# Performance work log

Measured on AMD Instinct MI355X. Metric: run time of the kernel, lower is better.

## Reference

```python
import jax, jax.numpy as jnp
import numpy as np

Q_MAX = 127.0  # 8-bit, narrow range [-127, 127] (pytorch-quantization default)


def fake_quant(x, amax):
    """Fake quantization with clipped-STE semantics (matches pytorch-quantization).

    amax may be a scalar (per-tensor) or broadcastable (per-channel). Treated as
    a constant (stop_gradient'd by caller where appropriate).
    """
    amax = jnp.maximum(amax, 1e-12)
    scale = amax / Q_MAX
    xq = jnp.round(jnp.clip(x / scale, -Q_MAX, Q_MAX)) * scale
    xc = jnp.clip(x, -amax, amax)  # identity grad inside range, zero outside
    return xc + jax.lax.stop_gradient(xq - xc)


def quant_conv1x1(x, w, b):
    """QuantConv2d with 1x1 kernel: fake-quant input (per-tensor dynamic max amax)
    and weight (per-output-channel max amax), then conv + bias.
    x: [B,C,H,W], w: [O,C], b: [O]
    """
    a_amax = jax.lax.stop_gradient(jnp.max(jnp.abs(x)))
    xq = fake_quant(x, a_amax)
    w_amax = jax.lax.stop_gradient(jnp.max(jnp.abs(w), axis=1, keepdims=True))
    wq = fake_quant(w, w_amax)
    y = jnp.einsum('bchw,oc->bohw', xq, wq)
    return y + b[None, :, None, None]


def setup_inputs() -> dict:
    key = jax.random.key(0)
    k1, k2, k3, k4 = jax.random.split(key, 4)
    B, C, Cr, H, W = 64, 32, 8, 128, 128
    x = jax.random.normal(k1, (B, C, H, W), dtype=jnp.float32)
    identity = jax.random.normal(k2, (B, C, H, W), dtype=jnp.float32)
    w_reduce = jax.random.normal(k3, (Cr, C), dtype=jnp.float32) * 0.1
    b_reduce = jnp.zeros((Cr,), dtype=jnp.float32)
    w_expand = jax.random.normal(k4, (C, Cr), dtype=jnp.float32) * 0.1
    b_expand = jnp.zeros((C,), dtype=jnp.float32)
    return {"x": x, "identity": identity,
            "w_reduce": w_reduce, "b_reduce": b_reduce,
            "w_expand": w_expand, "b_expand": b_expand}


def reference(x, identity, w_reduce, b_reduce, w_expand, b_expand):
    h = quant_conv1x1(x, w_reduce, b_reduce)      # [B,8,H,W]
    h = h * jax.nn.sigmoid(h)                     # SiLU
    g = quant_conv1x1(h, w_expand, b_expand)      # [B,32,H,W]
    return identity * jax.nn.sigmoid(g)
```

## Files before the change

### kernel.cpp

```cpp
#include <hip/hip_runtime.h>
#include <hip/hip_cooperative_groups.h>
#include <math.h>

namespace cg = cooperative_groups;

#define QMAX 127.0f
#define CIN 32
#define CR 8
#define HW 16384
#define BATCH 64
#define NPIX (BATCH*HW)
#define NQUAD (NPIX/4)
#define NX (BATCH*CIN*HW)
#define COOP_BLOCKS (NQUAD/256)

#define H_OFF 64
#define WS_NEEDED ((size_t)(H_OFF + (size_t)NPIX * CR) * 4)

__device__ __forceinline__ float fq(float v, float inv_scale, float scale) {
    return rintf(fminf(fmaxf(v * inv_scale, -QMAX), QMAX)) * scale;
}
__device__ __forceinline__ float sigmoidf_(float v) {
    return __builtin_amdgcn_rcpf(1.0f + __expf(-v));
}

__global__ __launch_bounds__(256, 4) void se_fused(const float* __restrict__ x,
                                                   const float* __restrict__ identity,
                                                   const float* __restrict__ wr,
                                                   const float* __restrict__ br,
                                                   const float* __restrict__ we,
                                                   const float* __restrict__ be,
                                                   unsigned int* __restrict__ wsu,
                                                   float* __restrict__ out) {
    cg::grid_group grid = cg::this_grid();
    int t = threadIdx.x;
    __shared__ float wqr[CR * CIN], wqe[CIN * CR], bsh[CR], besh[CIN], amr[CR], ame[CIN];
    __shared__ float red[4];

    if (t < CR) {
        float mm = 0.f;
        for (int c = 0; c < CIN; c++) mm = fmaxf(mm, fabsf(wr[t * CIN + c]));
        amr[t] = fmaxf(mm, 1e-12f);
        bsh[t] = br[t];
    }
    if (t >= 64 && t < 64 + CIN) {
        int r = t - 64;
        float mm = 0.f;
        for (int c = 0; c < CR; c++) mm = fmaxf(mm, fabsf(we[r * CR + c]));
        ame[r] = fmaxf(mm, 1e-12f);
        besh[r] = be[r];
    }
    __syncthreads();
    {
        float a1 = amr[t >> 5];
        wqr[t] = fq(wr[t], QMAX / a1, a1 * (1.f / QMAX));
        float a2 = ame[t >> 3];
        wqe[t] = fq(we[t], QMAX / a2, a2 * (1.f / QMAX));
    }
    __syncthreads();

    const int tid = blockIdx.x * 256 + t;

    {
        const float4* x4 = (const float4*)x;
        float m = 0.f;
#pragma unroll 8
        for (int i = 0; i < 32; i++) {
            float4 v = x4[tid + i * NQUAD];
            m = fmaxf(m, fmaxf(fmaxf(fabsf(v.x), fabsf(v.y)), fmaxf(fabsf(v.z), fabsf(v.w))));
        }
#pragma unroll
        for (int off = 32; off > 0; off >>= 1) m = fmaxf(m, __shfl_xor(m, off, 64));
        if ((t & 63) == 0) red[t >> 6] = m;
        __syncthreads();
        if (t == 0) {
            m = fmaxf(fmaxf(red[0], red[1]), fmaxf(red[2], red[3]));
            atomicMax(&wsu[0], __float_as_uint(m));
        }
    }
    grid.sync();

    float a_amax = fmaxf(__uint_as_float(
        __hip_atomic_load(&wsu[0], __ATOMIC_ACQUIRE, __HIP_MEMORY_SCOPE_AGENT)), 1e-12f);
    float ascale = a_amax * (1.f / QMAX), ainv = QMAX / a_amax;
    const int b = tid >> 12;
    const int hw = (tid & 4095) << 2;
    const size_t base = (size_t)b * CIN * HW + hw;
    float h[CR][4];
    {
        float hacc[CR][4];
#pragma unroll
        for (int o = 0; o < CR; o++)
#pragma unroll
            for (int v = 0; v < 4; v++) hacc[o][v] = 0.f;
        const float* xb = x + base;
#pragma unroll
        for (int c = 0; c < CIN; c++) {
            float4 xv = *(const float4*)(xb + (size_t)c * HW);
            float q0 = fq(xv.x, ainv, ascale), q1 = fq(xv.y, ainv, ascale);
            float q2 = fq(xv.z, ainv, ascale), q3 = fq(xv.w, ainv, ascale);
#pragma unroll
            for (int o = 0; o < CR; o++) {
                float w = wqr[o * CIN + c];
                hacc[o][0] += q0 * w; hacc[o][1] += q1 * w;
                hacc[o][2] += q2 * w; hacc[o][3] += q3 * w;
            }
        }
        float m = 0.f;
#pragma unroll
        for (int o = 0; o < CR; o++) {
            float bb = bsh[o];
#pragma unroll
            for (int v = 0; v < 4; v++) {
                float hv = hacc[o][v] + bb;
                hv = hv * sigmoidf_(hv);
                h[o][v] = hv;
                m = fmaxf(m, fabsf(hv));
            }
        }
#pragma unroll
        for (int off = 32; off > 0; off >>= 1) m = fmaxf(m, __shfl_xor(m, off, 64));
        __syncthreads();
        if ((t & 63) == 0) red[t >> 6] = m;
        __syncthreads();
        if (t == 0) {
            m = fmaxf(fmaxf(red[0], red[1]), fmaxf(red[2], red[3]));
            atomicMax(&wsu[1], __float_as_uint(m));
        }
    }
    grid.sync();

    float h_amax = fmaxf(__uint_as_float(
        __hip_atomic_load(&wsu[1], __ATOMIC_ACQUIRE, __HIP_MEMORY_SCOPE_AGENT)), 1e-12f);
    float hscale = h_amax * (1.f / QMAX), hinv = QMAX / h_amax;
#pragma unroll
    for (int o = 0; o < CR; o++)
#pragma unroll
        for (int v = 0; v < 4; v++) h[o][v] = fq(h[o][v], hinv, hscale);

#pragma unroll 4
    for (int o2 = 0; o2 < CIN; o2++) {
        float g0 = besh[o2], g1 = g0, g2 = g0, g3 = g0;
#pragma unroll
        for (int cr = 0; cr < CR; cr++) {
            float w = wqe[o2 * CR + cr];
            g0 += h[cr][0] * w; g1 += h[cr][1] * w;
            g2 += h[cr][2] * w; g3 += h[cr][3] * w;
        }
        size_t off = base + (size_t)o2 * HW;
        float4 idv = *(const float4*)(identity + off);
        float4 ov;
        ov.x = idv.x * sigmoidf_(g0);
        ov.y = idv.y * sigmoidf_(g1);
        ov.z = idv.z * sigmoidf_(g2);
        ov.w = idv.w * sigmoidf_(g3);
        *(float4*)(out + off) = ov;
    }
}

__global__ __launch_bounds__(256) void k1_xmax(const float4* __restrict__ x4,
                                               unsigned int* __restrict__ wsu) {
    int idx = blockIdx.x * 256 + threadIdx.x;
    float m = 0.f;
#pragma unroll
    for (int i = 0; i < 16; i++) {
        float4 v = x4[idx + i * 524288];
        m = fmaxf(m, fmaxf(fmaxf(fabsf(v.x), fabsf(v.y)), fmaxf(fabsf(v.z), fabsf(v.w))));
    }
#pragma unroll
    for (int off = 32; off > 0; off >>= 1) m = fmaxf(m, __shfl_xor(m, off, 64));
    __shared__ float red[4];
    int t = threadIdx.x;
    if ((t & 63) == 0) red[t >> 6] = m;
    __syncthreads();
    if (t == 0) {
        m = fmaxf(fmaxf(red[0], red[1]), fmaxf(red[2], red[3]));
        atomicMax(&wsu[0], __float_as_uint(m));
    }
}

__global__ __launch_bounds__(256) void k2_hmax(const float* __restrict__ x,
                                               const float* __restrict__ wr,
                                               const float* __restrict__ br,
                                               const unsigned int* __restrict__ wsu,
                                               unsigned int* __restrict__ hmax,
                                               float* __restrict__ hbuf) {
    __shared__ float wq[CR * CIN], bsh[CR], amr[CR];
    int t = threadIdx.x;
    if (t < CR) {
        float mm = 0.f;
        for (int c = 0; c < CIN; c++) mm = fmaxf(mm, fabsf(wr[t * CIN + c]));
        amr[t] = fmaxf(mm, 1e-12f);
        bsh[t] = br[t];
    }
    __syncthreads();
    {
        float amax = amr[t >> 5];
        wq[t] = fq(wr[t], QMAX / amax, amax * (1.f / QMAX));
    }
    __syncthreads();
    float a_amax = fmaxf(__uint_as_float(wsu[0]), 1e-12f);
    float scale = a_amax * (1.f / QMAX), inv_scale = QMAX / a_amax;
    int tid = blockIdx.x * 256 + t;
    int b = tid >> 12;
    int hw = (tid & 4095) << 2;
    const float* xb = x + (size_t)b * CIN * HW + hw;
    float hacc[CR][4];
#pragma unroll
    for (int o = 0; o < CR; o++)
#pragma unroll
        for (int v = 0; v < 4; v++) hacc[o][v] = 0.f;
#pragma unroll
    for (int c = 0; c < CIN; c++) {
        float4 xv = *(const float4*)(xb + (size_t)c * HW);
        float q0 = fq(xv.x, inv_scale, scale), q1 = fq(xv.y, inv_scale, scale);
        float q2 = fq(xv.z, inv_scale, scale), q3 = fq(xv.w, inv_scale, scale);
#pragma unroll
        for (int o = 0; o < CR; o++) {
            float w = wq[o * CIN + c];
            hacc[o][0] += q0 * w; hacc[o][1] += q1 * w;
            hacc[o][2] += q2 * w; hacc[o][3] += q3 * w;
        }
    }
    float m = 0.f;
#pragma unroll
    for (int o = 0; o < CR; o++) {
        float bb = bsh[o];
        float4 hv;
        float* hp = (float*)&hv;
#pragma unroll
        for (int v = 0; v < 4; v++) {
            float h = hacc[o][v] + bb;
            h = h * sigmoidf_(h);
            hp[v] = h;
            m = fmaxf(m, fabsf(h));
        }
        if (hbuf) *(float4*)(hbuf + ((size_t)(b * CR + o)) * HW + hw) = hv;
    }
#pragma unroll
    for (int off = 32; off > 0; off >>= 1) m = fmaxf(m, __shfl_xor(m, off, 64));
    __shared__ float red[4];
    if ((t & 63) == 0) red[t >> 6] = m;
    __syncthreads();
    if (t == 0) {
        m = fmaxf(fmaxf(red[0], red[1]), fmaxf(red[2], red[3]));
        atomicMax(hmax, __float_as_uint(m));
    }
}

__global__ __launch_bounds__(256) void k3_out(const float* __restrict__ hbuf,
                                              const float* __restrict__ identity,
                                              const float* __restrict__ we,
                                              const float* __restrict__ be,
                                              const unsigned int* __restrict__ wsu,
                                              float* __restrict__ out) {
    const int y = blockIdx.y;
    __shared__ float wqe[16 * CR], besh[16], ame[16];
    int t = threadIdx.x;
    if (t < 16) {
        int r = 16 * y + t;
        float mm = 0.f;
        for (int c = 0; c < CR; c++) mm = fmaxf(mm, fabsf(we[r * CR + c]));
        ame[t] = fmaxf(mm, 1e-12f);
        besh[t] = be[r];
    }
    __syncthreads();
    if (t < 128) {
        int r16 = t >> 3;
        float amax = ame[r16];
        wqe[t] = fq(we[(16 * y + r16) * CR + (t & 7)], QMAX / amax, amax * (1.f / QMAX));
    }
    __syncthreads();
    float h_amax = fmaxf(__uint_as_float(wsu[1]), 1e-12f);
    float hscale = h_amax * (1.f / QMAX), hinv = QMAX / h_amax;
    int tid = blockIdx.x * 256 + t;
    int b = tid >> 12;
    int hw = (tid & 4095) << 2;
    size_t base = (size_t)b * CIN * HW + hw;
    float hq[CR][4];
#pragma unroll
    for (int cr = 0; cr < CR; cr++) {
        float4 hv = *(const float4*)(hbuf + ((size_t)(b * CR + cr)) * HW + hw);
        hq[cr][0] = fq(hv.x, hinv, hscale);
        hq[cr][1] = fq(hv.y, hinv, hscale);
        hq[cr][2] = fq(hv.z, hinv, hscale);
        hq[cr][3] = fq(hv.w, hinv, hscale);
    }
#pragma unroll 4
    for (int o = 0; o < 16; o++) {
        float g0 = besh[o], g1 = g0, g2 = g0, g3 = g0;
#pragma unroll
        for (int cr = 0; cr < CR; cr++) {
            float w = wqe[o * CR + cr];
            g0 += hq[cr][0] * w; g1 += hq[cr][1] * w;
            g2 += hq[cr][2] * w; g3 += hq[cr][3] * w;
        }
        size_t off = base + (size_t)(16 * y + o) * HW;
        float4 idv = *(const float4*)(identity + off);
        float4 ov;
        ov.x = idv.x * sigmoidf_(g0);
        ov.y = idv.y * sigmoidf_(g1);
        ov.z = idv.z * sigmoidf_(g2);
        ov.w = idv.w * sigmoidf_(g3);
        *(float4*)(out + off) = ov;
    }
}

__global__ __launch_bounds__(256) void k3_out_rc(const float* __restrict__ x,
                                                 const float* __restrict__ identity,
                                                 const float* __restrict__ wr,
                                                 const float* __restrict__ br,
                                                 const float* __restrict__ we,
                                                 const float* __restrict__ be,
                                                 const unsigned int* __restrict__ wsu,
                                                 float* __restrict__ out) {
    __shared__ float wqr[CR * CIN], wqe[CIN * CR], bsh[CR], besh[CIN], amr[CR], ame[CIN];
    int t = threadIdx.x;
    if (t < CR) {
        float mm = 0.f;
        for (int c = 0; c < CIN; c++) mm = fmaxf(mm, fabsf(wr[t * CIN + c]));
        amr[t] = fmaxf(mm, 1e-12f);
        bsh[t] = br[t];
    }
    if (t >= 64 && t < 64 + CIN) {
        int r = t - 64;
        float mm = 0.f;
        for (int c = 0; c < CR; c++) mm = fmaxf(mm, fabsf(we[r * CR + c]));
        ame[r] = fmaxf(mm, 1e-12f);
        besh[r] = be[r];
    }
    __syncthreads();
    {
        float amax = amr[t >> 5];
        wqr[t] = fq(wr[t], QMAX / amax, amax * (1.f / QMAX));
        float amax2 = ame[t >> 3];
        wqe[t] = fq(we[t], QMAX / amax2, amax2 * (1.f / QMAX));
    }
    __syncthreads();
    float a_amax = fmaxf(__uint_as_float(wsu[0]), 1e-12f);
    float ascale = a_amax * (1.f / QMAX), ainv = QMAX / a_amax;
    float h_amax = fmaxf(__uint_as_float(wsu[1]), 1e-12f);
    float hscale = h_amax * (1.f / QMAX), hinv = QMAX / h_amax;
    int tid = blockIdx.x * 256 + t;
    int b = tid >> 12;
    int hw = (tid & 4095) << 2;
    size_t base = (size_t)b * CIN * HW + hw;
    const float* xb = x + base;
    float hq[CR][4];
    {
        float hacc[CR][4];
#pragma unroll
        for (int o = 0; o < CR; o++)
#pragma unroll
            for (int v = 0; v < 4; v++) hacc[o][v] = 0.f;
#pragma unroll
        for (int c = 0; c < CIN; c++) {
            float4 xv = *(const float4*)(xb + (size_t)c * HW);
            float q0 = fq(xv.x, ainv, ascale), q1 = fq(xv.y, ainv, ascale);
            float q2 = fq(xv.z, ainv, ascale), q3 = fq(xv.w, ainv, ascale);
#pragma unroll
            for (int o = 0; o < CR; o++) {
                float w = wqr[o * CIN + c];
                hacc[o][0] += q0 * w; hacc[o][1] += q1 * w;
                hacc[o][2] += q2 * w; hacc[o][3] += q3 * w;
            }
        }
#pragma unroll
        for (int o = 0; o < CR; o++) {
            float bb = bsh[o];
#pragma unroll
            for (int v = 0; v < 4; v++) {
                float h = hacc[o][v] + bb;
                h = h * sigmoidf_(h);
                hq[o][v] = fq(h, hinv, hscale);
            }
        }
    }
#pragma unroll 4
    for (int o2 = 0; o2 < CIN; o2++) {
        float g0 = besh[o2], g1 = g0, g2 = g0, g3 = g0;
#pragma unroll
        for (int cr = 0; cr < CR; cr++) {
            float w = wqe[o2 * CR + cr];
            g0 += hq[cr][0] * w; g1 += hq[cr][1] * w;
            g2 += hq[cr][2] * w; g3 += hq[cr][3] * w;
        }
        size_t off = base + (size_t)o2 * HW;
        float4 idv = *(const float4*)(identity + off);
        float4 ov;
        ov.x = idv.x * sigmoidf_(g0);
        ov.y = idv.y * sigmoidf_(g1);
        ov.z = idv.z * sigmoidf_(g2);
        ov.w = idv.w * sigmoidf_(g3);
        *(float4*)(out + off) = ov;
    }
}

extern "C" void kernel_launch(void* const* d_in, const int* in_sizes, int n_in,
                              void* d_out, int out_size, void* d_ws, size_t ws_size,
                              hipStream_t stream) {
    const float* x        = (const float*)d_in[0];
    const float* identity = (const float*)d_in[1];
    const float* wr       = (const float*)d_in[2];
    const float* br       = (const float*)d_in[3];
    const float* we       = (const float*)d_in[4];
    const float* be       = (const float*)d_in[5];
    float* out            = (float*)d_out;
    float* wsf            = (float*)d_ws;
    unsigned int* wsu     = (unsigned int*)d_ws;

    hipMemsetAsync(d_ws, 0, 16, stream);

    int maxb = 0;
    hipError_t qerr = hipOccupancyMaxActiveBlocksPerMultiprocessor(&maxb, se_fused, 256, 0);
    bool coop_ok = false;
    if (qerr == hipSuccess && maxb >= 4) {
        void* args[] = {(void*)&x, (void*)&identity, (void*)&wr, (void*)&br,
                        (void*)&we, (void*)&be, (void*)&wsu, (void*)&out};
        hipError_t lerr = hipLaunchCooperativeKernel((void*)se_fused, dim3(COOP_BLOCKS),
                                                     dim3(256), args, 0, stream);
        coop_ok = (lerr == hipSuccess);
    }
    if (coop_ok) return;

    const bool big_ws = (ws_size >= WS_NEEDED);
    float* hbuf = big_ws ? (wsf + H_OFF) : nullptr;
    hipLaunchKernelGGL(k1_xmax, dim3(2048), dim3(256), 0, stream, (const float4*)x, wsu);
    hipLaunchKernelGGL(k2_hmax, dim3(NQUAD / 256), dim3(256), 0, stream,
                       x, wr, br, wsu, &wsu[1], hbuf);
    if (big_ws) {
        hipLaunchKernelGGL(k3_out, dim3(NQUAD / 256, 2), dim3(256), 0, stream,
                           hbuf, identity, we, be, wsu, out);
    } else {
        hipLaunchKernelGGL(k3_out_rc, dim3(NQUAD / 256), dim3(256), 0, stream,
                           x, identity, wr, br, we, be, wsu, out);
    }
}
```

Measured before the change: 374.6 us.

## Replace cooperative fused kernel with three-kernel pipeline using batched loads and nontemporal IO

Removes the cooperative single-kernel path with two grid syncs and always runs the three-kernel path (x max, h compute/max, output). Each kernel now issues its global loads in a batch behind a scheduling barrier to raise memory-level parallelism. Threads cover two pixels instead of four, which doubles the grid. The output kernel handles all 32 channels in one block and uses nontemporal loads for identity and nontemporal stores for out. In exchange it pays for extra launches and an h round trip through the workspace.

```diff
diff --git a/kernel.cpp b/kernel.cpp
--- a/kernel.cpp
+++ b/kernel.cpp
@@ -1,8 +1,5 @@
 #include <hip/hip_runtime.h>
-#include <hip/hip_cooperative_groups.h>
 #include <math.h>
-
-namespace cg = cooperative_groups;
 
 #define QMAX 127.0f
 #define CIN 32
@@ -10,163 +7,41 @@
 #define HW 16384
 #define BATCH 64
 #define NPIX (BATCH*HW)
+#define NPAIR (NPIX/2)
 #define NQUAD (NPIX/4)
 #define NX (BATCH*CIN*HW)
-#define COOP_BLOCKS (NQUAD/256)
 
 #define H_OFF 64
 #define WS_NEEDED ((size_t)(H_OFF + (size_t)NPIX * CR) * 4)
 
+typedef float v2f __attribute__((ext_vector_type(2)));
+
 __device__ __forceinline__ float fq(float v, float inv_scale, float scale) {
     return rintf(fminf(fmaxf(v * inv_scale, -QMAX), QMAX)) * scale;
 }
 __device__ __forceinline__ float sigmoidf_(float v) {
     return __builtin_amdgcn_rcpf(1.0f + __expf(-v));
 }
-
-__global__ __launch_bounds__(256, 4) void se_fused(const float* __restrict__ x,
-                                                   const float* __restrict__ identity,
-                                                   const float* __restrict__ wr,
-                                                   const float* __restrict__ br,
-                                                   const float* __restrict__ we,
-                                                   const float* __restrict__ be,
-                                                   unsigned int* __restrict__ wsu,
-                                                   float* __restrict__ out) {
-    cg::grid_group grid = cg::this_grid();
-    int t = threadIdx.x;
-    __shared__ float wqr[CR * CIN], wqe[CIN * CR], bsh[CR], besh[CIN], amr[CR], ame[CIN];
-    __shared__ float red[4];
-
-    if (t < CR) {
-        float mm = 0.f;
-        for (int c = 0; c < CIN; c++) mm = fmaxf(mm, fabsf(wr[t * CIN + c]));
-        amr[t] = fmaxf(mm, 1e-12f);
-        bsh[t] = br[t];
-    }
-    if (t >= 64 && t < 64 + CIN) {
-        int r = t - 64;
-        float mm = 0.f;
-        for (int c = 0; c < CR; c++) mm = fmaxf(mm, fabsf(we[r * CR + c]));
-        ame[r] = fmaxf(mm, 1e-12f);
-        besh[r] = be[r];
-    }
-    __syncthreads();
-    {
-        float a1 = amr[t >> 5];
-        wqr[t] = fq(wr[t], QMAX / a1, a1 * (1.f / QMAX));
-        float a2 = ame[t >> 3];
-        wqe[t] = fq(we[t], QMAX / a2, a2 * (1.f / QMAX));
-    }
-    __syncthreads();
-
-    const int tid = blockIdx.x * 256 + t;
-
-    {
-        const float4* x4 = (const float4*)x;
-        float m = 0.f;
-#pragma unroll 8
-        for (int i = 0; i < 32; i++) {
-            float4 v = x4[tid + i * NQUAD];
-            m = fmaxf(m, fmaxf(fmaxf(fabsf(v.x), fabsf(v.y)), fmaxf(fabsf(v.z), fabsf(v.w))));
-        }
-#pragma unroll
-        for (int off = 32; off > 0; off >>= 1) m = fmaxf(m, __shfl_xor(m, off, 64));
-        if ((t & 63) == 0) red[t >> 6] = m;
-        __syncthreads();
-        if (t == 0) {
-            m = fmaxf(fmaxf(red[0], red[1]), fmaxf(red[2], red[3]));
-            atomicMax(&wsu[0], __float_as_uint(m));
-        }
-    }
-    grid.sync();
-
-    float a_amax = fmaxf(__uint_as_float(
-        __hip_atomic_load(&wsu[0], __ATOMIC_ACQUIRE, __HIP_MEMORY_SCOPE_AGENT)), 1e-12f);
-    float ascale = a_amax * (1.f / QMAX), ainv = QMAX / a_amax;
-    const int b = tid >> 12;
-    const int hw = (tid & 4095) << 2;
-    const size_t base = (size_t)b * CIN * HW + hw;
-    float h[CR][4];
-    {
-        float hacc[CR][4];
-#pragma unroll
-        for (int o = 0; o < CR; o++)
-#pragma unroll
-            for (int v = 0; v < 4; v++) hacc[o][v] = 0.f;
-        const float* xb = x + base;
-#pragma unroll
-        for (int c = 0; c < CIN; c++) {
-            float4 xv = *(const float4*)(xb + (size_t)c * HW);
-            float q0 = fq(xv.x, ainv, ascale), q1 = fq(xv.y, ainv, ascale);
-            float q2 = fq(xv.z, ainv, ascale), q3 = fq(xv.w, ainv, ascale);
-#pragma unroll
-            for (int o = 0; o < CR; o++) {
-                float w = wqr[o * CIN + c];
-                hacc[o][0] += q0 * w; hacc[o][1] += q1 * w;
-                hacc[o][2] += q2 * w; hacc[o][3] += q3 * w;
-            }
-        }
-        float m = 0.f;
-#pragma unroll
-        for (int o = 0; o < CR; o++) {
-            float bb = bsh[o];
-#pragma unroll
-            for (int v = 0; v < 4; v++) {
-                float hv = hacc[o][v] + bb;
-                hv = hv * sigmoidf_(hv);
-                h[o][v] = hv;
-                m = fmaxf(m, fabsf(hv));
-            }
-        }
-#pragma unroll
-        for (int off = 32; off > 0; off >>= 1) m = fmaxf(m, __shfl_xor(m, off, 64));
-        __syncthreads();
-        if ((t & 63) == 0) red[t >> 6] = m;
-        __syncthreads();
-        if (t == 0) {
-            m = fmaxf(fmaxf(red[0], red[1]), fmaxf(red[2], red[3]));
-            atomicMax(&wsu[1], __float_as_uint(m));
-        }
-    }
-    grid.sync();
-
-    float h_amax = fmaxf(__uint_as_float(
-        __hip_atomic_load(&wsu[1], __ATOMIC_ACQUIRE, __HIP_MEMORY_SCOPE_AGENT)), 1e-12f);
-    float hscale = h_amax * (1.f / QMAX), hinv = QMAX / h_amax;
-#pragma unroll
-    for (int o = 0; o < CR; o++)
-#pragma unroll
-        for (int v = 0; v < 4; v++) h[o][v] = fq(h[o][v], hinv, hscale);
-
-#pragma unroll 4
-    for (int o2 = 0; o2 < CIN; o2++) {
-        float g0 = besh[o2], g1 = g0, g2 = g0, g3 = g0;
-#pragma unroll
-        for (int cr = 0; cr < CR; cr++) {
-            float w = wqe[o2 * CR + cr];
-            g0 += h[cr][0] * w; g1 += h[cr][1] * w;
-            g2 += h[cr][2] * w; g3 += h[cr][3] * w;
-        }
-        size_t off = base + (size_t)o2 * HW;
-        float4 idv = *(const float4*)(identity + off);
-        float4 ov;
-        ov.x = idv.x * sigmoidf_(g0);
-        ov.y = idv.y * sigmoidf_(g1);
-        ov.z = idv.z * sigmoidf_(g2);
-        ov.w = idv.w * sigmoidf_(g3);
-        *(float4*)(out + off) = ov;
-    }
+__device__ __forceinline__ v2f nt_load2(const float* p) {
+    return __builtin_nontemporal_load((const v2f*)p);
+}
+__device__ __forceinline__ void nt_store2(float* p, float a, float b) {
+    v2f v; v.x = a; v.y = b;
+    __builtin_nontemporal_store(v, (v2f*)p);
 }
 
 __global__ __launch_bounds__(256) void k1_xmax(const float4* __restrict__ x4,
                                                unsigned int* __restrict__ wsu) {
     int idx = blockIdx.x * 256 + threadIdx.x;
+    float4 v[8];
+#pragma unroll
+    for (int i = 0; i < 8; i++) v[i] = x4[idx + i * 1048576];
+    __builtin_amdgcn_sched_barrier(0);
     float m = 0.f;
 #pragma unroll
-    for (int i = 0; i < 16; i++) {
-        float4 v = x4[idx + i * 524288];
-        m = fmaxf(m, fmaxf(fmaxf(fabsf(v.x), fabsf(v.y)), fmaxf(fabsf(v.z), fabsf(v.w))));
-    }
+    for (int i = 0; i < 8; i++)
+        m = fmaxf(m, fmaxf(fmaxf(fabsf(v[i].x), fabsf(v[i].y)),
+                           fmaxf(fabsf(v[i].z), fabsf(v[i].w))));
 #pragma unroll
     for (int off = 32; off > 0; off >>= 1) m = fmaxf(m, __shfl_xor(m, off, 64));
     __shared__ float red[4];
@@ -200,42 +75,53 @@
     }
     __syncthreads();
     float a_amax = fmaxf(__uint_as_float(wsu[0]), 1e-12f);
-    float scale = a_amax * (1.f / QMAX), inv_scale = QMAX / a_amax;
+    float ascale = a_amax * (1.f / QMAX), ainv = QMAX / a_amax;
+
     int tid = blockIdx.x * 256 + t;
-    int b = tid >> 12;
-    int hw = (tid & 4095) << 2;
+    int b = tid >> 13;
+    int hw = (tid & 8191) << 1;
     const float* xb = x + (size_t)b * CIN * HW + hw;
-    float hacc[CR][4];
-#pragma unroll
-    for (int o = 0; o < CR; o++)
-#pragma unroll
-        for (int v = 0; v < 4; v++) hacc[o][v] = 0.f;
-#pragma unroll
-    for (int c = 0; c < CIN; c++) {
-        float4 xv = *(const float4*)(xb + (size_t)c * HW);
-        float q0 = fq(xv.x, inv_scale, scale), q1 = fq(xv.y, inv_scale, scale);
-        float q2 = fq(xv.z, inv_scale, scale), q3 = fq(xv.w, inv_scale, scale);
-#pragma unroll
-        for (int o = 0; o < CR; o++) {
-            float w = wq[o * CIN + c];
-            hacc[o][0] += q0 * w; hacc[o][1] += q1 * w;
-            hacc[o][2] += q2 * w; hacc[o][3] += q3 * w;
-        }
-    }
+
+    float hacc[CR][2];
+#pragma unroll
+    for (int o = 0; o < CR; o++) { hacc[o][0] = 0.f; hacc[o][1] = 0.f; }
+
+#pragma unroll
+    for (int s = 0; s < 2; s++) {
+        float2 xv[16];
+#pragma unroll
+        for (int j = 0; j < 16; j++)
+            xv[j] = *(const float2*)(xb + (size_t)(s * 16 + j) * HW);
+        __builtin_amdgcn_sched_barrier(0);
+#pragma unroll
+        for (int j4 = 0; j4 < 4; j4++) {
+            float q0[4], q1[4];
+#pragma unroll
+            for (int k = 0; k < 4; k++) {
+                q0[k] = fq(xv[j4 * 4 + k].x, ainv, ascale);
+                q1[k] = fq(xv[j4 * 4 + k].y, ainv, ascale);
+            }
+            int c0 = s * 16 + j4 * 4;
+#pragma unroll
+            for (int o = 0; o < CR; o++) {
+                float4 wv = *(const float4*)&wq[o * CIN + c0];
+                hacc[o][0] += q0[0]*wv.x + q0[1]*wv.y + q0[2]*wv.z + q0[3]*wv.w;
+                hacc[o][1] += q1[0]*wv.x + q1[1]*wv.y + q1[2]*wv.z + q1[3]*wv.w;
+            }
+        }
+    }
+
     float m = 0.f;
 #pragma unroll
     for (int o = 0; o < CR; o++) {
         float bb = bsh[o];
-        float4 hv;
-        float* hp = (float*)&hv;
-#pragma unroll
-        for (int v = 0; v < 4; v++) {
-            float h = hacc[o][v] + bb;
-            h = h * sigmoidf_(h);
-            hp[v] = h;
-            m = fmaxf(m, fabsf(h));
-        }
-        if (hbuf) *(float4*)(hbuf + ((size_t)(b * CR + o)) * HW + hw) = hv;
+        float h0 = hacc[o][0] + bb; h0 = h0 * sigmoidf_(h0);
+        float h1 = hacc[o][1] + bb; h1 = h1 * sigmoidf_(h1);
+        m = fmaxf(m, fmaxf(fabsf(h0), fabsf(h1)));
+        if (hbuf) {
+            float2 hv; hv.x = h0; hv.y = h1;
+            *(float2*)(hbuf + (size_t)(b * CR + o) * HW + hw) = hv;
+        }
     }
 #pragma unroll
     for (int off = 32; off > 0; off >>= 1) m = fmaxf(m, __shfl_xor(m, off, 64));
@@ -254,55 +140,61 @@
                                               const float* __restrict__ be,
                                               const unsigned int* __restrict__ wsu,
                                               float* __restrict__ out) {
-    const int y = blockIdx.y;
-    __shared__ float wqe[16 * CR], besh[16], ame[16];
+    __shared__ float wqe[CIN * CR], besh[CIN], ame[CIN];
     int t = threadIdx.x;
-    if (t < 16) {
-        int r = 16 * y + t;
+    if (t < CIN) {
         float mm = 0.f;
-        for (int c = 0; c < CR; c++) mm = fmaxf(mm, fabsf(we[r * CR + c]));
+        for (int c = 0; c < CR; c++) mm = fmaxf(mm, fabsf(we[t * CR + c]));
         ame[t] = fmaxf(mm, 1e-12f);
-        besh[t] = be[r];
-    }
-    __syncthreads();
-    if (t < 128) {
-        int r16 = t >> 3;
-        float amax = ame[r16];
-        wqe[t] = fq(we[(16 * y + r16) * CR + (t & 7)], QMAX / amax, amax * (1.f / QMAX));
+        besh[t] = be[t];
+    }
+    __syncthreads();
+    {
+        float amax = ame[t >> 3];
+        wqe[t] = fq(we[t], QMAX / amax, amax * (1.f / QMAX));
     }
     __syncthreads();
     float h_amax = fmaxf(__uint_as_float(wsu[1]), 1e-12f);
     float hscale = h_amax * (1.f / QMAX), hinv = QMAX / h_amax;
+
     int tid = blockIdx.x * 256 + t;
-    int b = tid >> 12;
-    int hw = (tid & 4095) << 2;
-    size_t base = (size_t)b * CIN * HW + hw;
-    float hq[CR][4];
+    int b = tid >> 13;
+    int hw = (tid & 8191) << 1;
+
+    float2 hv[CR];
+#pragma unroll
+    for (int cr = 0; cr < CR; cr++)
+        hv[cr] = *(const float2*)(hbuf + (size_t)(b * CR + cr) * HW + hw);
+    __builtin_amdgcn_sched_barrier(0);
+    float hq0[CR], hq1[CR];
 #pragma unroll
     for (int cr = 0; cr < CR; cr++) {
-        float4 hv = *(const float4*)(hbuf + ((size_t)(b * CR + cr)) * HW + hw);
-        hq[cr][0] = fq(hv.x, hinv, hscale);
-        hq[cr][1] = fq(hv.y, hinv, hscale);
-        hq[cr][2] = fq(hv.z, hinv, hscale);
-        hq[cr][3] = fq(hv.w, hinv, hscale);
-    }
-#pragma unroll 4
-    for (int o = 0; o < 16; o++) {
-        float g0 = besh[o], g1 = g0, g2 = g0, g3 = g0;
-#pragma unroll
-        for (int cr = 0; cr < CR; cr++) {
-            float w = wqe[o * CR + cr];
-            g0 += hq[cr][0] * w; g1 += hq[cr][1] * w;
-            g2 += hq[cr][2] * w; g3 += hq[cr][3] * w;
-        }
-        size_t off = base + (size_t)(16 * y + o) * HW;
-        float4 idv = *(const float4*)(identity + off);
-        float4 ov;
-        ov.x = idv.x * sigmoidf_(g0);
-        ov.y = idv.y * sigmoidf_(g1);
-        ov.z = idv.z * sigmoidf_(g2);
-        ov.w = idv.w * sigmoidf_(g3);
-        *(float4*)(out + off) = ov;
+        hq0[cr] = fq(hv[cr].x, hinv, hscale);
+        hq1[cr] = fq(hv[cr].y, hinv, hscale);
+    }
+
+    const size_t base = (size_t)b * CIN * HW + hw;
+#pragma unroll
+    for (int og = 0; og < 4; og++) {
+        v2f idv[8];
+#pragma unroll
+        for (int j = 0; j < 8; j++)
+            idv[j] = nt_load2(identity + base + (size_t)(og * 8 + j) * HW);
+        __builtin_amdgcn_sched_barrier(0);
+#pragma unroll
+        for (int j = 0; j < 8; j++) {
+            int o2 = og * 8 + j;
+            float4 w0 = *(const float4*)&wqe[o2 * CR];
+            float4 w1 = *(const float4*)&wqe[o2 * CR + 4];
+            float g0 = besh[o2]
+                + hq0[0]*w0.x + hq0[1]*w0.y + hq0[2]*w0.z + hq0[3]*w0.w
+                + hq0[4]*w1.x + hq0[5]*w1.y + hq0[6]*w1.z + hq0[7]*w1.w;
+            float g1 = besh[o2]
+                + hq1[0]*w0.x + hq1[1]*w0.y + hq1[2]*w0.z + hq1[3]*w0.w
+                + hq1[4]*w1.x + hq1[5]*w1.y + hq1[6]*w1.z + hq1[7]*w1.w;
+            nt_store2(out + base + (size_t)o2 * HW,
+                      idv[j].x * sigmoidf_(g0), idv[j].y * sigmoidf_(g1));
+        }
     }
 }
 
@@ -411,25 +303,14 @@
 
     hipMemsetAsync(d_ws, 0, 16, stream);
 
-    int maxb = 0;
-    hipError_t qerr = hipOccupancyMaxActiveBlocksPerMultiprocessor(&maxb, se_fused, 256, 0);
-    bool coop_ok = false;
-    if (qerr == hipSuccess && maxb >= 4) {
-        void* args[] = {(void*)&x, (void*)&identity, (void*)&wr, (void*)&br,
-                        (void*)&we, (void*)&be, (void*)&wsu, (void*)&out};
-        hipError_t lerr = hipLaunchCooperativeKernel((void*)se_fused, dim3(COOP_BLOCKS),
-                                                     dim3(256), args, 0, stream);
-        coop_ok = (lerr == hipSuccess);
-    }
-    if (coop_ok) return;
-
     const bool big_ws = (ws_size >= WS_NEEDED);
     float* hbuf = big_ws ? (wsf + H_OFF) : nullptr;
-    hipLaunchKernelGGL(k1_xmax, dim3(2048), dim3(256), 0, stream, (const float4*)x, wsu);
-    hipLaunchKernelGGL(k2_hmax, dim3(NQUAD / 256), dim3(256), 0, stream,
+
+    hipLaunchKernelGGL(k1_xmax, dim3(4096), dim3(256), 0, stream, (const float4*)x, wsu);
+    hipLaunchKernelGGL(k2_hmax, dim3(NPAIR / 256), dim3(256), 0, stream,
                        x, wr, br, wsu, &wsu[1], hbuf);
     if (big_ws) {
-        hipLaunchKernelGGL(k3_out, dim3(NQUAD / 256, 2), dim3(256), 0, stream,
+        hipLaunchKernelGGL(k3_out, dim3(NPAIR / 256), dim3(256), 0, stream,
                            hbuf, identity, we, be, wsu, out);
     } else {
         hipLaunchKernelGGL(k3_out_rc, dim3(NQUAD / 256), dim3(256), 0, stream,
```

Result: no change. 371.7 us (-0.8%).
